# Optimization experiments

Hardware: AMD Instinct MI355X
Metric: run time of the kernel (lower is better)

## Reference

```python
import jax, jax.numpy as jnp
import numpy as np

DEPTH = 5
B, CHANNELS, LENGTH = 256, 10, 128


def setup_inputs() -> dict:
    key = jax.random.key(0)
    # torch module convention: (batch, channels, length); transposed internally to (length, channels)
    path = jax.random.normal(key, (B, CHANNELS, LENGTH), dtype=jnp.float32)
    return {"path": path, "depth": DEPTH}


def _seg_levels(delta, depth):
    # Signature of a single linear segment with increment delta: level k = delta^{\otimes k} / k!
    # delta: (B, d) -> list of (B, d**k) for k = 1..depth
    b = delta.shape[0]
    levels = [delta]
    cur = delta
    for k in range(2, depth + 1):
        cur = (cur[:, :, None] * delta[:, None, :]).reshape(b, -1) / k
        levels.append(cur)
    return levels


def _signature(path_ld, depth):
    # path_ld: (B, L, d) piecewise-linear path; returns (B, sum_k d**k)
    b, L, d = path_ld.shape
    inc = path_ld[:, 1:] - path_ld[:, :-1]  # (B, L-1, d) segment increments
    init = tuple(_seg_levels(inc[:, 0], depth))

    def step(carry, delta):
        # Chen's relation: (S \otimes T)_k = S_k + T_k + sum_{i=1}^{k-1} S_i \otimes T_{k-i}
        T = _seg_levels(delta, depth)
        new = []
        for k in range(1, depth + 1):
            acc = carry[k - 1] + T[k - 1]
            for i in range(1, k):
                acc = acc + (carry[i - 1][:, :, None] * T[k - i - 1][:, None, :]).reshape(b, d ** k)
            new.append(acc)
        return tuple(new), None

    deltas = jnp.swapaxes(inc[:, 1:], 0, 1)  # (L-2, B, d) remaining segments
    final, _ = jax.lax.scan(step, init, deltas)
    return jnp.concatenate(final, axis=-1)


def reference(path, depth):
    # path: (B, channels, length) as in the torch module; iisignature sees (length, channels)
    return _signature(jnp.swapaxes(path, 1, 2), depth)
```

## Files before the change

### kernel.cpp

```cpp
#include <hip/hip_runtime.h>


#define D10    10
#define LPATH  128
#define NSEG   127
#define BLOCK  256
#define KC     16
#define RS     12
#define OUT_PER_B 111110

__global__ __launch_bounds__(BLOCK) void sig_kernel(
        const float* __restrict__ path,
        float* __restrict__ out)
{
    __shared__ __align__(16) float dT[NSEG * RS];
    __shared__ float Wp1[KC * 100];
    __shared__ float Wp0[KC * 100];

    const int tid = threadIdx.x;
    const int bb  = blockIdx.x;
    const int b   = bb / 10;
    const int g   = bb - b * 10;
    const float* pb = path + (size_t)b * (D10 * LPATH);

    for (int idx = tid; idx < NSEG * D10; idx += BLOCK) {
        int t = idx / D10, c = idx - t * D10;
        dT[t * RS + c] = pb[c * LPATH + t + 1] - pb[c * LPATH + t];
    }

    const int c2 = tid / 10;
    const int c3 = tid - c2 * 10;
    int m3r[4];
#pragma unroll
    for (int r = 0; r < 4; r++) m3r[r] = (tid + 250 * r) / 10;

    float s1 = 0.f, s2 = 0.f, s3 = 0.f;
    float S4r[4] = {0.f, 0.f, 0.f, 0.f};
    float acc[4][10];
#pragma unroll
    for (int r = 0; r < 4; r++)
#pragma unroll
        for (int e = 0; e < 10; e++) acc[r][e] = 0.f;

    for (int kc0 = 0; kc0 < NSEG; kc0 += KC) {
        const int kn = (NSEG - kc0 < KC) ? (NSEG - kc0) : KC;
        __syncthreads();

        if (tid < 100) {
            for (int kl = 0; kl < kn; kl++) {
                const int t = kc0 + kl;
                float dg  = dT[t * RS + g];
                float dc2 = dT[t * RS + c2];
                float dc3 = dT[t * RS + c3];
                float u24 = s2 + (s1 + dg * 0.25f)       * dc2 * (1.f / 3.f);
                float u25 = s2 + (s1 + dg * 0.2f)        * dc2 * 0.25f;
                float u23 = s2 + (s1 + dg * (1.f / 3.f)) * dc2 * 0.5f;
                Wp1[kl * 100 + tid] = s3 + u24 * dc3 * 0.5f;
                Wp0[kl * 100 + tid] = s3 + u25 * dc3 * (1.f / 3.f);
                s3 += u23 * dc3;
                s2 += (s1 + dg * 0.5f) * dc2;
                s1 += dg;
            }
        }
        __syncthreads();

        if (tid < 250) {
            for (int kl = 0; kl < kn; kl++) {
                const int t = kc0 + kl;
                const float* dr = &dT[t * RS];
                float4 dA = *(const float4*)dr;
                float4 dB = *(const float4*)(dr + 4);
                float2 dC = *(const float2*)(dr + 8);
                float de[10] = {dA.x, dA.y, dA.z, dA.w,
                                dB.x, dB.y, dB.z, dB.w, dC.x, dC.y};
                float dc4v = dr[c3];
                float hd   = 0.5f * dc4v;
#pragma unroll
                for (int r = 0; r < 4; r++) {
                    float w1v = Wp1[kl * 100 + m3r[r]];
                    float w0v = Wp0[kl * 100 + m3r[r]];
                    float c4v = S4r[r] + w0v * hd;
                    S4r[r] += w1v * dc4v;
#pragma unroll
                    for (int e = 0; e < 10; e++) acc[r][e] += c4v * de[e];
                }
            }
        }
    }

    float* ob = out + (size_t)b * OUT_PER_B;
    if (tid < 100) {
        ob[110 + g * 100 + tid] = s3;
        if (c3 == 0) ob[10 + g * 10 + c2] = s2;
        if (tid == 0) ob[g] = s1;
    }
    if (tid < 250) {
#pragma unroll
        for (int r = 0; r < 4; r++) {
            const int j = tid + 250 * r;
            ob[1110 + g * 1000 + j] = S4r[r];
            float* o5 = ob + 11110 + (size_t)g * 10000 + (size_t)j * 10;
#pragma unroll
            for (int e = 0; e < 10; e += 2) {
                float2 vv = make_float2(acc[r][e], acc[r][e + 1]);
                *(float2*)&o5[e] = vv;
            }
        }
    }
}

extern "C" void kernel_launch(void* const* d_in, const int* in_sizes, int n_in,
                              void* d_out, int out_size, void* d_ws, size_t ws_size,
                              hipStream_t stream) {
    const float* path = (const float*)d_in[0];
    float* out = (float*)d_out;
    int B = in_sizes[0] / (D10 * LPATH);
    sig_kernel<<<B * 10, BLOCK, 0, stream>>>(path, out);
}
```

Measured before the change: 231.5 us.

## Restructure signature kernel so each thread owns full level-3 prefix with 100 accumulators

Each thread now owns one (g,c2,c3) level-3 index and computes levels 1-3 itself, redundantly. It accumulates all 100 level-5 and 10 level-4 entries in registers, so the two-phase producer/consumer scheme through shared memory and the per-chunk barriers go away. Blocks now cover 5 first-level channels with 512 threads instead of 1 channel with 256, and the time loop is software-pipelined with double-buffered loads. This removes synchronisation and wasted idle threads but raises register pressure (about 110+ live accumulators) and cuts the grid from 2560 to 512 blocks.

```diff
diff --git a/kernel.cpp b/kernel.cpp
--- a/kernel.cpp
+++ b/kernel.cpp
@@ -4,108 +4,105 @@
 #define D10    10
 #define LPATH  128
 #define NSEG   127
-#define BLOCK  256
-#define KC     16
 #define RS     12
+#define BLOCK  512
 #define OUT_PER_B 111110
 
-__global__ __launch_bounds__(BLOCK) void sig_kernel(
+__global__ __launch_bounds__(BLOCK, 2) void sig_kernel(
         const float* __restrict__ path,
         float* __restrict__ out)
 {
-    __shared__ __align__(16) float dT[NSEG * RS];
-    __shared__ float Wp1[KC * 100];
-    __shared__ float Wp0[KC * 100];
+    __shared__ __align__(16) float dT[(NSEG + 1) * RS];
 
     const int tid = threadIdx.x;
     const int bb  = blockIdx.x;
-    const int b   = bb / 10;
-    const int g   = bb - b * 10;
+    const int b   = bb >> 1;
+    const int gh  = (bb & 1) * 5;
     const float* pb = path + (size_t)b * (D10 * LPATH);
 
     for (int idx = tid; idx < NSEG * D10; idx += BLOCK) {
         int t = idx / D10, c = idx - t * D10;
         dT[t * RS + c] = pb[c * LPATH + t + 1] - pb[c * LPATH + t];
     }
+    if (tid < RS) dT[NSEG * RS + tid] = 0.f;
 
-    const int c2 = tid / 10;
-    const int c3 = tid - c2 * 10;
-    int m3r[4];
-#pragma unroll
-    for (int r = 0; r < 4; r++) m3r[r] = (tid + 250 * r) / 10;
+    const int gg = tid / 100;
+    const int m3 = tid - gg * 100;
+    const int g  = gh + gg;
+    const int c2 = m3 / 10;
+    const int c3 = m3 - c2 * 10;
 
     float s1 = 0.f, s2 = 0.f, s3 = 0.f;
-    float S4r[4] = {0.f, 0.f, 0.f, 0.f};
-    float acc[4][10];
+    float S4[D10];
+    float acc[D10][D10];
 #pragma unroll
-    for (int r = 0; r < 4; r++)
+    for (int i = 0; i < D10; ++i) {
+        S4[i] = 0.f;
 #pragma unroll
-        for (int e = 0; e < 10; e++) acc[r][e] = 0.f;
-
-    for (int kc0 = 0; kc0 < NSEG; kc0 += KC) {
-        const int kn = (NSEG - kc0 < KC) ? (NSEG - kc0) : KC;
-        __syncthreads();
-
-        if (tid < 100) {
-            for (int kl = 0; kl < kn; kl++) {
-                const int t = kc0 + kl;
-                float dg  = dT[t * RS + g];
-                float dc2 = dT[t * RS + c2];
-                float dc3 = dT[t * RS + c3];
-                float u24 = s2 + (s1 + dg * 0.25f)       * dc2 * (1.f / 3.f);
-                float u25 = s2 + (s1 + dg * 0.2f)        * dc2 * 0.25f;
-                float u23 = s2 + (s1 + dg * (1.f / 3.f)) * dc2 * 0.5f;
-                Wp1[kl * 100 + tid] = s3 + u24 * dc3 * 0.5f;
-                Wp0[kl * 100 + tid] = s3 + u25 * dc3 * (1.f / 3.f);
-                s3 += u23 * dc3;
-                s2 += (s1 + dg * 0.5f) * dc2;
-                s1 += dg;
-            }
-        }
-        __syncthreads();
-
-        if (tid < 250) {
-            for (int kl = 0; kl < kn; kl++) {
-                const int t = kc0 + kl;
-                const float* dr = &dT[t * RS];
-                float4 dA = *(const float4*)dr;
-                float4 dB = *(const float4*)(dr + 4);
-                float2 dC = *(const float2*)(dr + 8);
-                float de[10] = {dA.x, dA.y, dA.z, dA.w,
-                                dB.x, dB.y, dB.z, dB.w, dC.x, dC.y};
-                float dc4v = dr[c3];
-                float hd   = 0.5f * dc4v;
-#pragma unroll
-                for (int r = 0; r < 4; r++) {
-                    float w1v = Wp1[kl * 100 + m3r[r]];
-                    float w0v = Wp0[kl * 100 + m3r[r]];
-                    float c4v = S4r[r] + w0v * hd;
-                    S4r[r] += w1v * dc4v;
-#pragma unroll
-                    for (int e = 0; e < 10; e++) acc[r][e] += c4v * de[e];
-                }
-            }
-        }
+        for (int e = 0; e < D10; ++e) acc[i][e] = 0.f;
     }
 
-    float* ob = out + (size_t)b * OUT_PER_B;
-    if (tid < 100) {
-        ob[110 + g * 100 + tid] = s3;
+    __syncthreads();
+
+    if (tid < 500) {
+        auto load = [&](float (&de)[D10], float &dg, float &d2, float &d3, int t) {
+            const float* dr = &dT[t * RS];
+            float4 A  = *(const float4*)dr;
+            float4 Bv = *(const float4*)(dr + 4);
+            float2 Cv = *(const float2*)(dr + 8);
+            de[0] = A.x;  de[1] = A.y;  de[2] = A.z;  de[3] = A.w;
+            de[4] = Bv.x; de[5] = Bv.y; de[6] = Bv.z; de[7] = Bv.w;
+            de[8] = Cv.x; de[9] = Cv.y;
+            dg = dr[g]; d2 = dr[c2]; d3 = dr[c3];
+        };
+        auto step = [&](const float (&de)[D10], float dg, float d2, float d3) {
+            float u24 = s2 + (s1 + dg * 0.25f)       * d2 * (1.f / 3.f);
+            float u25 = s2 + (s1 + dg * 0.2f)        * d2 * 0.25f;
+            float u23 = s2 + (s1 + dg * (1.f / 3.f)) * d2 * 0.5f;
+            float w1  = s3 + u24 * d3 * 0.5f;
+            float w0  = s3 + u25 * d3 * (1.f / 3.f);
+            s3 += u23 * d3;
+            s2 += (s1 + dg * 0.5f) * d2;
+            s1 += dg;
+            float w0h = 0.5f * w0;
+#pragma unroll
+            for (int c4 = 0; c4 < D10; ++c4) {
+                float dcv = de[c4];
+                float c4v = fmaf(w0h, dcv, S4[c4]);
+                S4[c4] = fmaf(w1, dcv, S4[c4]);
+#pragma unroll
+                for (int e = 0; e < D10; ++e)
+                    acc[c4][e] = fmaf(c4v, de[e], acc[c4][e]);
+            }
+        };
+
+        float deA[D10], deB[D10];
+        float dgA, d2A, d3A, dgB, d2B, d3B;
+        load(deA, dgA, d2A, d3A, 0);
+#pragma unroll 1
+        for (int t = 0; t + 2 <= NSEG; t += 2) {
+            load(deB, dgB, d2B, d3B, t + 1);
+            step(deA, dgA, d2A, d3A);
+            load(deA, dgA, d2A, d3A, t + 2);
+            step(deB, dgB, d2B, d3B);
+        }
+        step(deA, dgA, d2A, d3A);
+
+        float* ob = out + (size_t)b * OUT_PER_B;
+        if (m3 == 0) ob[g] = s1;
         if (c3 == 0) ob[10 + g * 10 + c2] = s2;
-        if (tid == 0) ob[g] = s1;
-    }
-    if (tid < 250) {
+        ob[110 + g * 100 + m3] = s3;
+        float* o4 = ob + 1110 + g * 1000 + m3 * 10;
 #pragma unroll
-        for (int r = 0; r < 4; r++) {
-            const int j = tid + 250 * r;
-            ob[1110 + g * 1000 + j] = S4r[r];
-            float* o5 = ob + 11110 + (size_t)g * 10000 + (size_t)j * 10;
+        for (int e = 0; e < D10; e += 2)
+            *(float2*)&o4[e] = make_float2(S4[e], S4[e + 1]);
+        float* o5 = ob + 11110 + (size_t)g * 10000 + (size_t)m3 * 100;
 #pragma unroll
-            for (int e = 0; e < 10; e += 2) {
-                float2 vv = make_float2(acc[r][e], acc[r][e + 1]);
-                *(float2*)&o5[e] = vv;
-            }
-        }
+        for (int c4 = 0; c4 < D10; ++c4)
+#pragma unroll
+            for (int e = 0; e < D10; e += 2)
+                *(float2*)&o5[c4 * 10 + e] =
+                    make_float2(acc[c4][e], acc[c4][e + 1]);
     }
 }
 
@@ -115,5 +112,5 @@
     const float* path = (const float*)d_in[0];
     float* out = (float*)d_out;
     int B = in_sizes[0] / (D10 * LPATH);
-    sig_kernel<<<B * 10, BLOCK, 0, stream>>>(path, out);
+    sig_kernel<<<B * 2, BLOCK, 0, stream>>>(path, out);
 }
```

Result: faster. 218.3 us (-5.7%).

## Recast level-4/5 signature accumulation as split-bf16 MFMA matrix products

Applied to the files above, without the earlier changes.

Level-4 and level-5 terms become a GEMM over time segments. Each block builds an A matrix of level-3 weights (rows of 250 index triples) and a B matrix of increment products, using the suffix sums of increments. These are multiplied with bf16 MFMA instructions, using a hi/lo split (four MFMAs per tile) to keep near-fp32 accuracy. This replaces the scalar FMA loops, and the grid changes to 4 blocks of 512 threads per batch. The cost is padding to 256x112 tiles, extra MFMA passes for the precision split, and more complex strided output writes.

```diff
diff --git a/kernel.cpp b/kernel.cpp
--- a/kernel.cpp
+++ b/kernel.cpp
@@ -4,106 +4,195 @@
 #define D10    10
 #define LPATH  128
 #define NSEG   127
-#define BLOCK  256
+#define BLOCK  512
+#define NROW   256
+#define NROWA  250
+#define NCOL   112
+#define NCOLA  110
 #define KC     16
-#define RS     12
+#define NCH    8
+#define SD     132
 #define OUT_PER_B 111110
 
-__global__ __launch_bounds__(BLOCK) void sig_kernel(
+typedef __attribute__((ext_vector_type(8))) short bf16x8;
+typedef __attribute__((ext_vector_type(4))) float f32x4;
+
+__device__ __forceinline__ unsigned pack_split(float x, float y, unsigned &lo)
+{
+    unsigned xb = __float_as_uint(x), yb = __float_as_uint(y);
+    float xr = x - __uint_as_float(xb & 0xffff0000u);
+    float yr = y - __uint_as_float(yb & 0xffff0000u);
+    lo = (__float_as_uint(xr) >> 16) | (__float_as_uint(yr) & 0xffff0000u);
+    return (xb >> 16) | (yb & 0xffff0000u);
+}
+
+__global__ __launch_bounds__(BLOCK, 2) void sig_kernel(
         const float* __restrict__ path,
         float* __restrict__ out)
 {
-    __shared__ __align__(16) float dT[NSEG * RS];
-    __shared__ float Wp1[KC * 100];
-    __shared__ float Wp0[KC * 100];
+    __shared__ __align__(16) float dTT[D10 * SD];
+    __shared__ __align__(16) float RT [D10 * SD];
+    __shared__ __align__(16) short Ahi[4 * NROW * 8];
+    __shared__ __align__(16) short Alo[4 * NROW * 8];
+    __shared__ __align__(16) short Bhi[4 * NCOL * 8];
+    __shared__ __align__(16) short Blo[4 * NCOL * 8];
 
     const int tid = threadIdx.x;
     const int bb  = blockIdx.x;
-    const int b   = bb / 10;
-    const int g   = bb - b * 10;
+    const int b   = bb >> 2;
+    const int q   = bb & 3;
     const float* pb = path + (size_t)b * (D10 * LPATH);
 
-    for (int idx = tid; idx < NSEG * D10; idx += BLOCK) {
-        int t = idx / D10, c = idx - t * D10;
-        dT[t * RS + c] = pb[c * LPATH + t + 1] - pb[c * LPATH + t];
-    }
-
-    const int c2 = tid / 10;
-    const int c3 = tid - c2 * 10;
-    int m3r[4];
-#pragma unroll
-    for (int r = 0; r < 4; r++) m3r[r] = (tid + 250 * r) / 10;
+    for (int idx = tid; idx < D10 * SD; idx += BLOCK) {
+        int c = idx / SD, t = idx - c * SD;
+        float d = 0.f, r = 0.f;
+        if (t < NSEG) {
+            float p1 = pb[c * LPATH + t + 1];
+            d = p1 - pb[c * LPATH + t];
+            r = pb[c * LPATH + NSEG] - p1;
+        }
+        dTT[idx] = d;
+        RT [idx] = r;
+    }
+    for (int idx = tid; idx < 4 * (NROW - NROWA) * 8; idx += BLOCK) {
+        int kg = idx / ((NROW - NROWA) * 8);
+        int rem = idx - kg * ((NROW - NROWA) * 8);
+        int o = (kg * NROW + NROWA) * 8 + rem;
+        Ahi[o] = 0; Alo[o] = 0;
+    }
+    if (tid < 4 * 2 * 8) {
+        int kg = tid >> 4, rem = tid & 15;
+        int o = (kg * NCOL + NCOLA) * 8 + rem;
+        Bhi[o] = 0; Blo[o] = 0;
+    }
+
+    const int grow = q * NROWA + tid;
+    const int g   = grow / 100;
+    const int m3  = grow - g * 100;
+    const int c2  = m3 / 10;
+    const int c3  = m3 - c2 * 10;
+    const int goff = g * SD, c2off = c2 * SD, c3off = c3 * SD;
+
+    const int cb  = tid >> 2;
+    const int kgB = tid & 3;
+    int c4o = 0, ebo = 0;
+    if (cb < 100) { int c4 = cb / 10; ebo = (cb - c4 * 10) * SD; c4o = c4 * SD; }
+    else          { c4o = (cb - 100) * SD; }
+
+    const int lane = tid & 63;
+    const int wv   = tid >> 6;
+    const int rl   = lane & 15;
+    const int kgl  = lane >> 4;
 
     float s1 = 0.f, s2 = 0.f, s3 = 0.f;
-    float S4r[4] = {0.f, 0.f, 0.f, 0.f};
-    float acc[4][10];
-#pragma unroll
-    for (int r = 0; r < 4; r++)
-#pragma unroll
-        for (int e = 0; e < 10; e++) acc[r][e] = 0.f;
-
-    for (int kc0 = 0; kc0 < NSEG; kc0 += KC) {
-        const int kn = (NSEG - kc0 < KC) ? (NSEG - kc0) : KC;
+    f32x4 acc[2][7];
+#pragma unroll
+    for (int i = 0; i < 2; ++i)
+#pragma unroll
+        for (int nt = 0; nt < 7; ++nt) acc[i][nt] = f32x4{0.f, 0.f, 0.f, 0.f};
+
+    __syncthreads();
+
+    for (int ch = 0; ch < NCH; ++ch) {
+        const int kc0 = ch * KC;
+        if (tid < NROWA) {
+#pragma unroll
+            for (int w0 = 0; w0 < KC; w0 += 4) {
+                float4 g4 = *(const float4*)&dTT[goff  + kc0 + w0];
+                float4 a4 = *(const float4*)&dTT[c2off + kc0 + w0];
+                float4 b4 = *(const float4*)&dTT[c3off + kc0 + w0];
+                float ga[4] = {g4.x, g4.y, g4.z, g4.w};
+                float aa[4] = {a4.x, a4.y, a4.z, a4.w};
+                float ba[4] = {b4.x, b4.y, b4.z, b4.w};
+                unsigned hw[4], lw[4];
+#pragma unroll
+                for (int j = 0; j < 4; ++j) {
+                    float dg = ga[j], d2 = aa[j], d3 = ba[j];
+                    float u24 = s2 + (s1 + dg * 0.25f)     * d2 * (1.f / 3.f);
+                    float u25 = s2 + (s1 + dg * 0.2f)      * d2 * 0.25f;
+                    float u23 = s2 + (s1 + dg * (1.f/3.f)) * d2 * 0.5f;
+                    float w1v = s3 + u24 * d3 * 0.5f;
+                    float w0h = 0.5f * (s3 + u25 * d3 * (1.f / 3.f));
+                    s3 += u23 * d3;
+                    s2 += (s1 + dg * 0.5f) * d2;
+                    s1 += dg;
+                    hw[j] = pack_split(w1v, w0h, lw[j]);
+                }
+                const int ai = ((w0 >> 2) * NROW + tid) * 8;
+                *(uint4*)&Ahi[ai] = make_uint4(hw[0], hw[1], hw[2], hw[3]);
+                *(uint4*)&Alo[ai] = make_uint4(lw[0], lw[1], lw[2], lw[3]);
+            }
+        }
+        if (tid < 440) {
+            const int u0 = kc0 + kgB * 4;
+            float4 d4 = *(const float4*)&dTT[c4o + u0];
+            float da[4] = {d4.x, d4.y, d4.z, d4.w};
+            unsigned hw[4], lw[4];
+            if (cb < 100) {
+                float4 e4 = *(const float4*)&dTT[ebo + u0];
+                float4 r4 = *(const float4*)&RT [ebo + u0];
+                float ea[4] = {e4.x, e4.y, e4.z, e4.w};
+                float ra[4] = {r4.x, r4.y, r4.z, r4.w};
+#pragma unroll
+                for (int j = 0; j < 4; ++j)
+                    hw[j] = pack_split(da[j] * ra[j], da[j] * ea[j], lw[j]);
+            } else {
+#pragma unroll
+                for (int j = 0; j < 4; ++j)
+                    hw[j] = pack_split(da[j], 0.f, lw[j]);
+            }
+            const int bi = (kgB * NCOL + cb) * 8;
+            *(uint4*)&Bhi[bi] = make_uint4(hw[0], hw[1], hw[2], hw[3]);
+            *(uint4*)&Blo[bi] = make_uint4(lw[0], lw[1], lw[2], lw[3]);
+        }
         __syncthreads();
-
-        if (tid < 100) {
-            for (int kl = 0; kl < kn; kl++) {
-                const int t = kc0 + kl;
-                float dg  = dT[t * RS + g];
-                float dc2 = dT[t * RS + c2];
-                float dc3 = dT[t * RS + c3];
-                float u24 = s2 + (s1 + dg * 0.25f)       * dc2 * (1.f / 3.f);
-                float u25 = s2 + (s1 + dg * 0.2f)        * dc2 * 0.25f;
-                float u23 = s2 + (s1 + dg * (1.f / 3.f)) * dc2 * 0.5f;
-                Wp1[kl * 100 + tid] = s3 + u24 * dc3 * 0.5f;
-                Wp0[kl * 100 + tid] = s3 + u25 * dc3 * (1.f / 3.f);
-                s3 += u23 * dc3;
-                s2 += (s1 + dg * 0.5f) * dc2;
-                s1 += dg;
+        {
+            bf16x8 bh[7], bl[7];
+#pragma unroll
+            for (int nt = 0; nt < 7; ++nt) {
+                const int bi = (kgl * NCOL + nt * 16 + rl) * 8;
+                bh[nt] = *(const bf16x8*)&Bhi[bi];
+                bl[nt] = *(const bf16x8*)&Blo[bi];
+            }
+#pragma unroll
+            for (int i = 0; i < 2; ++i) {
+                const int ai = (kgl * NROW + wv * 32 + i * 16 + rl) * 8;
+                bf16x8 ah = *(const bf16x8*)&Ahi[ai];
+                bf16x8 al = *(const bf16x8*)&Alo[ai];
+#pragma unroll
+                for (int nt = 0; nt < 7; ++nt) {
+                    acc[i][nt] = __builtin_amdgcn_mfma_f32_16x16x32_bf16(ah, bh[nt], acc[i][nt], 0, 0, 0);
+                    acc[i][nt] = __builtin_amdgcn_mfma_f32_16x16x32_bf16(ah, bl[nt], acc[i][nt], 0, 0, 0);
+                    acc[i][nt] = __builtin_amdgcn_mfma_f32_16x16x32_bf16(al, bh[nt], acc[i][nt], 0, 0, 0);
+                    acc[i][nt] = __builtin_amdgcn_mfma_f32_16x16x32_bf16(al, bl[nt], acc[i][nt], 0, 0, 0);
+                }
             }
         }
         __syncthreads();
-
-        if (tid < 250) {
-            for (int kl = 0; kl < kn; kl++) {
-                const int t = kc0 + kl;
-                const float* dr = &dT[t * RS];
-                float4 dA = *(const float4*)dr;
-                float4 dB = *(const float4*)(dr + 4);
-                float2 dC = *(const float2*)(dr + 8);
-                float de[10] = {dA.x, dA.y, dA.z, dA.w,
-                                dB.x, dB.y, dB.z, dB.w, dC.x, dC.y};
-                float dc4v = dr[c3];
-                float hd   = 0.5f * dc4v;
-#pragma unroll
-                for (int r = 0; r < 4; r++) {
-                    float w1v = Wp1[kl * 100 + m3r[r]];
-                    float w0v = Wp0[kl * 100 + m3r[r]];
-                    float c4v = S4r[r] + w0v * hd;
-                    S4r[r] += w1v * dc4v;
-#pragma unroll
-                    for (int e = 0; e < 10; e++) acc[r][e] += c4v * de[e];
+    }
+
+    float* ob = out + (size_t)b * OUT_PER_B;
+    if (tid < NROWA) {
+        ob[110 + grow] = s3;
+        if (c3 == 0) ob[10 + g * 10 + c2] = s2;
+        if (m3 == 0) ob[g] = s1;
+    }
+#pragma unroll
+    for (int i = 0; i < 2; ++i) {
+#pragma unroll
+        for (int r = 0; r < 4; ++r) {
+            const int prow = wv * 32 + i * 16 + kgl * 4 + r;
+            if (prow < NROWA) {
+                const int gr = q * NROWA + prow;
+#pragma unroll
+                for (int nt = 0; nt < 7; ++nt) {
+                    const int col = nt * 16 + rl;
+                    const float v = acc[i][nt][r];
+                    if (col < 100)
+                        ob[11110 + (size_t)gr * 100 + col] = v;
+                    else if (col < NCOLA)
+                        ob[1110 + gr * 10 + (col - 100)] = v;
                 }
-            }
-        }
-    }
-
-    float* ob = out + (size_t)b * OUT_PER_B;
-    if (tid < 100) {
-        ob[110 + g * 100 + tid] = s3;
-        if (c3 == 0) ob[10 + g * 10 + c2] = s2;
-        if (tid == 0) ob[g] = s1;
-    }
-    if (tid < 250) {
-#pragma unroll
-        for (int r = 0; r < 4; r++) {
-            const int j = tid + 250 * r;
-            ob[1110 + g * 1000 + j] = S4r[r];
-            float* o5 = ob + 11110 + (size_t)g * 10000 + (size_t)j * 10;
-#pragma unroll
-            for (int e = 0; e < 10; e += 2) {
-                float2 vv = make_float2(acc[r][e], acc[r][e + 1]);
-                *(float2*)&o5[e] = vv;
             }
         }
     }
@@ -115,5 +204,5 @@
     const float* path = (const float*)d_in[0];
     float* out = (float*)d_out;
     int B = in_sizes[0] / (D10 * LPATH);
-    sig_kernel<<<B * 10, BLOCK, 0, stream>>>(path, out);
+    sig_kernel<<<B * 4, BLOCK, 0, stream>>>(path, out);
 }
```

Result: faster. 204.2 us (-11.8%).
